# Optimization experiments

Measured on AMD Instinct MI355X. Metric: run time of the kernel, lower is better.

The kernel has to match this reference:

```python
import jax, jax.numpy as jnp
import numpy as np

B, NHID, L, AL = 8, 512, 2048, 4
NHEAD, HEAD_DIM = 8, 64
D = NHEAD * HEAD_DIM
WIN = 3  # unfold_size in the original module
SCALE = 1.0 / float(np.sqrt(HEAD_DIM))


def setup_inputs() -> dict:
    key = jax.random.key(0)
    ks = jax.random.split(key, 6)
    s = 0.02
    return {
        "x": jax.random.normal(ks[0], (B, NHID, L, 1), jnp.float32),
        "ax": jax.random.normal(ks[1], (B, NHID, AL, L), jnp.float32),
        "Wq": jax.random.normal(ks[2], (NHID, D), jnp.float32) * s,
        "bq": jnp.zeros((D,), jnp.float32),
        "Wk": jax.random.normal(ks[3], (NHID, D), jnp.float32) * s,
        "bk": jnp.zeros((D,), jnp.float32),
        "Wv": jax.random.normal(ks[4], (NHID, D), jnp.float32) * s,
        "bv": jnp.zeros((D,), jnp.float32),
        "Wo": jax.random.normal(ks[5], (D, NHID), jnp.float32) * s,
        "bo": jnp.zeros((NHID,), jnp.float32),
    }


def _window_unfold(t):
    # SAME zero-padded sliding window of size 3 along L (== tf.image.extract_patches).
    tp = jnp.pad(t, ((0, 0), (0, 0), (0, 0), (1, 1)))
    Ld = t.shape[-1]
    return jnp.stack([tp[..., i:i + Ld] for i in range(WIN)], axis=3)


def reference(x, ax, Wq, bq, Wk, bk, Wv, bv, Wo, bo):
    # x: [B, nhid, L, 1] -> [B, L, nhid]
    xf = x[..., 0].transpose(0, 2, 1)
    q = (xf @ Wq + bq).transpose(0, 2, 1).reshape(B, NHEAD, HEAD_DIM, L)
    k = (xf @ Wk + bk).transpose(0, 2, 1).reshape(B, NHEAD, HEAD_DIM, L)
    v = (xf @ Wv + bv).transpose(0, 2, 1).reshape(B, NHEAD, HEAD_DIM, L)

    kw = _window_unfold(k)  # [B, nh, hd, 3, L]
    vw = _window_unfold(v)

    # axial context: ax [B, nhid, aL, L] -> [B, aL, L, nhid]
    axf = ax.transpose(0, 2, 3, 1)
    ak = (axf @ Wk + bk).transpose(0, 3, 1, 2).reshape(B, NHEAD, HEAD_DIM, AL, L)
    av = (axf @ Wv + bv).transpose(0, 3, 1, 2).reshape(B, NHEAD, HEAD_DIM, AL, L)

    kall = jnp.concatenate([kw, ak], axis=3)  # [B, nh, hd, 3+aL, L]
    vall = jnp.concatenate([vw, av], axis=3)

    # per-position attention over the (3 + aL) window entries
    scores = jnp.einsum('bndl,bndwl->bnwl', q, kall) * SCALE
    alphas = jax.nn.softmax(scores, axis=2)  # softmax over window dim (dropout omitted)
    att = jnp.einsum('bnwl,bndwl->bndl', alphas, vall).reshape(B, D, L)

    out = att.transpose(0, 2, 1) @ Wo + bo  # [B, L, nhid]
    return out.transpose(0, 2, 1)[..., None]  # [B, nhid, L, 1]
```

## Files before the change

kernel.cpp:

```cpp
#include <hip/hip_runtime.h>
#include <hip/hip_bf16.h>

#define B_ 8
#define NHID_ 512
#define L_ 2048
#define AL_ 4
#define NHEAD_ 8
#define HDIM_ 64
#define D_ 512
#define SCALE_ 0.125f

typedef unsigned short ushort_t;
typedef __attribute__((ext_vector_type(8))) short bf16x8;
typedef __attribute__((ext_vector_type(8))) unsigned short u16x8;
typedef __attribute__((ext_vector_type(4))) float f32x4;

__device__ __forceinline__ float bf2f(ushort_t u) {
  union { unsigned i; float f; } x; x.i = ((unsigned)u) << 16; return x.f;
}
__device__ __forceinline__ ushort_t f2bf(float f) {
  unsigned u = __float_as_uint(f);
  unsigned r = (u + 0x7FFFu + ((u >> 16) & 1u)) >> 16;
  return (ushort_t)r;
}
__device__ __forceinline__ void gload16(const ushort_t* g, ushort_t* l) {
  __builtin_amdgcn_global_load_lds(
      (const __attribute__((address_space(1))) unsigned int*)g,
      (__attribute__((address_space(3))) unsigned int*)l, 16, 0, 0);
}

template <typename Tin>
__global__ __launch_bounds__(256)
void transpose_conv(const Tin* __restrict__ in, ushort_t* __restrict__ out,
                    int R, int C) {
  __shared__ float t[32][33];
  const size_t z = (size_t)blockIdx.z * R * C;
  const int cb = blockIdx.x * 32, rb = blockIdx.y * 32;
  const int tx = threadIdx.x, ty = threadIdx.y;
#pragma unroll
  for (int i = 0; i < 4; i++) {
    const int r = rb + ty + i * 8;
    float v;
    if constexpr (sizeof(Tin) == 4) v = ((const float*)in)[z + (size_t)r * C + cb + tx];
    else                            v = bf2f(((const ushort_t*)in)[z + (size_t)r * C + cb + tx]);
    t[ty + i * 8][tx] = v;
  }
  __syncthreads();
#pragma unroll
  for (int i = 0; i < 4; i++) {
    const int c = cb + ty + i * 8;
    out[z + (size_t)c * R + rb + tx] = f2bf(t[tx][ty + i * 8]);
  }
}

__global__ void prep_bias(const float* __restrict__ bq, const float* __restrict__ bk,
                          const float* __restrict__ bv, float* __restrict__ bcat) {
  const int i = blockIdx.x * 256 + threadIdx.x;
  const float* s = i < 512 ? bq : (i < 1024 ? bk : bv);
  bcat[i] = s[i & 511];
}

template <int OUTF>
__global__ __launch_bounds__(256)
void gemm_mfma(const ushort_t* __restrict__ A, const ushort_t* __restrict__ W,
               const float* __restrict__ bias, void* __restrict__ C0,
               void* __restrict__ C1, void* __restrict__ C2,
               int Ntiles, int MbShift) {
  __shared__ ushort_t lds[8192];
  const int tid = threadIdx.x;
  const int l = tid & 63, w = tid >> 6;

  const int nwg = gridDim.x;
  const int id = (blockIdx.x & 7) * (nwg >> 3) + (blockIdx.x >> 3);
  const int nt = id % Ntiles, mt = id / Ntiles;
  const int bm = mt * 128, bn = nt * 128;

  const ushort_t* gsrc[4];
  ushort_t* ldst[4];
#pragma unroll
  for (int j = 0; j < 4; j++) {
    const int ci = j * 256 + w * 64 + l;
    const int row = (ci & 511) >> 2;
    const int cp = (ci & 3) ^ ((row >> 1) & 3);
    gsrc[j] = (ci < 512 ? A + (size_t)(bm + row) * 512
                        : W + (size_t)(bn + row) * 512) + cp * 8;
    ldst[j] = &lds[j * 2048 + w * 512];
  }

  const int wm = (w & 1) * 64, wn = (w >> 1) * 64;
  int boff[4], aoff[4];
#pragma unroll
  for (int i = 0; i < 4; i++) {
    const int rb = wm + i * 16 + (l & 15);
    boff[i] = rb * 32 + (((l >> 4) ^ ((rb >> 1) & 3)) * 8);
    const int ra = wn + i * 16 + (l & 15);
    aoff[i] = 4096 + ra * 32 + (((l >> 4) ^ ((ra >> 1) & 3)) * 8);
  }

  f32x4 acc[4][4] = {};
  for (int kt = 0; kt < 16; kt++) {
    if (kt) __syncthreads();
#pragma unroll
    for (int j = 0; j < 4; j++) gload16(gsrc[j] + kt * 32, ldst[j]);
    __syncthreads();
    bf16x8 bf[4], af[4];
#pragma unroll
    for (int i = 0; i < 4; i++) bf[i] = *(const bf16x8*)&lds[boff[i]];
#pragma unroll
    for (int i = 0; i < 4; i++) af[i] = *(const bf16x8*)&lds[aoff[i]];
#pragma unroll
    for (int ni = 0; ni < 4; ni++)
#pragma unroll
      for (int mi = 0; mi < 4; mi++)
        acc[ni][mi] = __builtin_amdgcn_mfma_f32_16x16x32_bf16(af[ni], bf[mi],
                                                              acc[ni][mi], 0, 0, 0);
  }

  const int bufi = bn >> 9;
  void* Cb = bufi == 0 ? C0 : (bufi == 1 ? C1 : C2);
  const int nb = bn & 511;
  const int Mb = 1 << MbShift;
#pragma unroll
  for (int ni = 0; ni < 4; ni++) {
#pragma unroll
    for (int r = 0; r < 4; r++) {
      const int tn = wn + ni * 16 + (l >> 4) * 4 + r;
      const float bv = bias[bn + tn];
      const int nl = nb + tn;
#pragma unroll
      for (int mi = 0; mi < 4; mi++) {
        const int m = bm + wm + mi * 16 + (l & 15);
        const int b = m >> MbShift, ml = m & (Mb - 1);
        const size_t idx = (((size_t)b * 512 + nl) << MbShift) + ml;
        const float val = acc[ni][mi][r] + bv;
        if (OUTF) ((float*)Cb)[idx] = val;
        else      ((ushort_t*)Cb)[idx] = f2bf(val);
      }
    }
  }
}

__global__ __launch_bounds__(256)
void attn_win(const ushort_t* __restrict__ q, const ushort_t* __restrict__ k,
              const ushort_t* __restrict__ v, const ushort_t* __restrict__ ak,
              const ushort_t* __restrict__ av, ushort_t* __restrict__ att,
              int b0) {
  const int lane = threadIdx.x & 63;
  const int w    = threadIdx.x >> 6;
  const int dc   = lane & 3;
  const int lc   = lane >> 2;
  const int bb = blockIdx.y >> 3, n = blockIdx.y & 7;
  const int b = b0 + bb;
  const int l8 = blockIdx.x * 512 + w * 128 + lc * 8;
  const int d0 = dc * 16;

  const size_t rq = ((size_t)b * D_ + n * HDIM_ + d0) * L_ + l8;
  const size_t ra = ((size_t)bb * D_ + n * HDIM_ + d0) * (size_t)(AL_ * L_) + l8;
  const ushort_t* qp = q + rq;
  const ushort_t* kp = k + rq;
  const ushort_t* vp = v + rq;
  ushort_t*       op = att + rq;
  const ushort_t* akp = ak + ra;
  const ushort_t* avp = av + ra;

  float s0[8] = {}, s1[8] = {}, s2[8] = {}, s3[8] = {};
  float s4[8] = {}, s5[8] = {}, s6[8] = {};

#pragma unroll 4
  for (int i = 0; i < 16; ++i) {
    const ushort_t* kr = kp + (size_t)i * L_;
    const ushort_t* ar = akp + (size_t)i * (AL_ * L_);
    const u16x8 qv = *(const u16x8*)(qp + (size_t)i * L_);
    const u16x8 kv = *(const u16x8*)kr;
    const u16x8 a0 = *(const u16x8*)(ar);
    const u16x8 a1 = *(const u16x8*)(ar + L_);
    const u16x8 a2 = *(const u16x8*)(ar + 2 * L_);
    const u16x8 a3 = *(const u16x8*)(ar + 3 * L_);
    float qf[8], kf[8];
#pragma unroll
    for (int j = 0; j < 8; ++j) { qf[j] = bf2f(qv[j]); kf[j] = bf2f(kv[j]); }
    float kl = __shfl_up(kf[7], 4);
    if (lc == 0) kl = (l8 > 0) ? bf2f(kr[-1]) : 0.f;
    float kh = __shfl_down(kf[0], 4);
    if (lc == 15) kh = (l8 + 8 < L_) ? bf2f(kr[8]) : 0.f;
#pragma unroll
    for (int j = 0; j < 8; ++j) {
      s0[j] = fmaf(qf[j], j ? kf[j - 1] : kl, s0[j]);
      s1[j] = fmaf(qf[j], kf[j], s1[j]);
      s2[j] = fmaf(qf[j], j < 7 ? kf[j + 1] : kh, s2[j]);
      s3[j] = fmaf(qf[j], bf2f(a0[j]), s3[j]);
      s4[j] = fmaf(qf[j], bf2f(a1[j]), s4[j]);
      s5[j] = fmaf(qf[j], bf2f(a2[j]), s5[j]);
      s6[j] = fmaf(qf[j], bf2f(a3[j]), s6[j]);
    }
  }

#pragma unroll
  for (int j = 0; j < 8; ++j) {
    s0[j] += __shfl_xor(s0[j], 1); s0[j] += __shfl_xor(s0[j], 2);
    s1[j] += __shfl_xor(s1[j], 1); s1[j] += __shfl_xor(s1[j], 2);
    s2[j] += __shfl_xor(s2[j], 1); s2[j] += __shfl_xor(s2[j], 2);
    s3[j] += __shfl_xor(s3[j], 1); s3[j] += __shfl_xor(s3[j], 2);
    s4[j] += __shfl_xor(s4[j], 1); s4[j] += __shfl_xor(s4[j], 2);
    s5[j] += __shfl_xor(s5[j], 1); s5[j] += __shfl_xor(s5[j], 2);
    s6[j] += __shfl_xor(s6[j], 1); s6[j] += __shfl_xor(s6[j], 2);
  }

#pragma unroll
  for (int j = 0; j < 8; ++j) {
    const float t0 = s0[j] * SCALE_, t1 = s1[j] * SCALE_, t2 = s2[j] * SCALE_;
    const float t3 = s3[j] * SCALE_, t4 = s4[j] * SCALE_, t5 = s5[j] * SCALE_;
    const float t6 = s6[j] * SCALE_;
    const float mx = fmaxf(fmaxf(fmaxf(t0, t1), fmaxf(t2, t3)),
                           fmaxf(fmaxf(t4, t5), t6));
    float e0 = __expf(t0 - mx), e1 = __expf(t1 - mx), e2 = __expf(t2 - mx);
    float e3 = __expf(t3 - mx), e4 = __expf(t4 - mx), e5 = __expf(t5 - mx);
    float e6 = __expf(t6 - mx);
    const float inv = 1.f / (e0 + e1 + e2 + e3 + e4 + e5 + e6);
    s0[j] = e0 * inv; s1[j] = e1 * inv; s2[j] = e2 * inv; s3[j] = e3 * inv;
    s4[j] = e4 * inv; s5[j] = e5 * inv; s6[j] = e6 * inv;
  }

#pragma unroll 4
  for (int i = 0; i < 16; ++i) {
    const ushort_t* vr = vp + (size_t)i * L_;
    const ushort_t* ar = avp + (size_t)i * (AL_ * L_);
    const u16x8 vv = *(const u16x8*)vr;
    const u16x8 a0 = *(const u16x8*)(ar);
    const u16x8 a1 = *(const u16x8*)(ar + L_);
    const u16x8 a2 = *(const u16x8*)(ar + 2 * L_);
    const u16x8 a3 = *(const u16x8*)(ar + 3 * L_);
    float vf[8];
#pragma unroll
    for (int j = 0; j < 8; ++j) vf[j] = bf2f(vv[j]);
    float vl = __shfl_up(vf[7], 4);
    if (lc == 0) vl = (l8 > 0) ? bf2f(vr[-1]) : 0.f;
    float vh = __shfl_down(vf[0], 4);
    if (lc == 15) vh = (l8 + 8 < L_) ? bf2f(vr[8]) : 0.f;
    u16x8 o;
#pragma unroll
    for (int j = 0; j < 8; ++j) {
      float r = s0[j] * (j ? vf[j - 1] : vl)
              + s1[j] * vf[j]
              + s2[j] * (j < 7 ? vf[j + 1] : vh);
      r = fmaf(s3[j], bf2f(a0[j]), r);
      r = fmaf(s4[j], bf2f(a1[j]), r);
      r = fmaf(s5[j], bf2f(a2[j]), r);
      r = fmaf(s6[j], bf2f(a3[j]), r);
      o[j] = f2bf(r);
    }
    *(u16x8*)(op + (size_t)i * L_) = o;
  }
}

extern "C" void kernel_launch(void* const* d_in, const int* in_sizes, int n_in,
                              void* d_out, int out_size, void* d_ws, size_t ws_size,
                              hipStream_t stream) {
  const float* x  = (const float*)d_in[0];
  const float* ax = (const float*)d_in[1];
  const float* Wq = (const float*)d_in[2];
  const float* bq = (const float*)d_in[3];
  const float* Wk = (const float*)d_in[4];
  const float* bk = (const float*)d_in[5];
  const float* Wv = (const float*)d_in[6];
  const float* bv = (const float*)d_in[7];
  const float* Wo = (const float*)d_in[8];
  const float* bo = (const float*)d_in[9];
  float* out = (float*)d_out;

  const size_t E  = (size_t)B_ * D_ * L_;
  const size_t EA = (size_t)B_ * D_ * AL_ * L_;
  const size_t CH1 = (size_t)D_ * AL_ * L_;
  const size_t wfix = 1536 * 512 + 512 * 512 + 3072;

  int BCH = 8;
  while (BCH > 1 &&
         (4 * E + EA + 2 * (size_t)BCH * CH1 + wfix) * 2 > ws_size)
    BCH >>= 1;
  const size_t chunkE = (size_t)BCH * CH1;

  ushort_t* wsu = (ushort_t*)d_ws;
  ushort_t* xTb   = wsu;
  ushort_t* qb    = xTb + E;
  ushort_t* kb    = qb + E;
  ushort_t* vb    = kb + E;
  ushort_t* axTb  = vb + E;
  ushort_t* akb   = axTb + EA;
  ushort_t* avb   = akb + chunkE;
  ushort_t* WcatT = avb + chunkE;
  ushort_t* WoT   = WcatT + 1536 * 512;
  float*    bcat  = (float*)(WoT + 512 * 512);
  ushort_t* attb  = xTb;
  ushort_t* attTb = axTb;

  const dim3 t32x8(32, 8);

  transpose_conv<float><<<dim3(16, 16, 1), t32x8, 0, stream>>>(Wq, WcatT, 512, 512);
  transpose_conv<float><<<dim3(16, 16, 1), t32x8, 0, stream>>>(Wk, WcatT + 512 * 512, 512, 512);
  transpose_conv<float><<<dim3(16, 16, 1), t32x8, 0, stream>>>(Wv, WcatT + 1024 * 512, 512, 512);
  transpose_conv<float><<<dim3(16, 16, 1), t32x8, 0, stream>>>(Wo, WoT, 512, 512);
  prep_bias<<<dim3(6), dim3(256), 0, stream>>>(bq, bk, bv, bcat);

  transpose_conv<float><<<dim3(64, 16, B_), t32x8, 0, stream>>>(x, xTb, 512, L_);
  transpose_conv<float><<<dim3(256, 16, B_), t32x8, 0, stream>>>(ax, axTb, 512, AL_ * L_);

  gemm_mfma<0><<<dim3(128 * 12), dim3(256), 0, stream>>>(
      xTb, WcatT, bcat, qb, kb, vb, 12, 11);

  for (int b0 = 0; b0 < B_; b0 += BCH) {
    const ushort_t* axc = axTb + (size_t)b0 * CH1;
    gemm_mfma<0><<<dim3(BCH * 64 * 8), dim3(256), 0, stream>>>(
        axc, WcatT + 512 * 512, bcat + 512, akb, avb, nullptr, 8, 13);
    attn_win<<<dim3(L_ / 512, BCH * NHEAD_), dim3(256), 0, stream>>>(
        qb, kb, vb, akb, avb, attb, b0);
  }

  transpose_conv<ushort_t><<<dim3(64, 16, B_), t32x8, 0, stream>>>(attb, attTb, 512, L_);

  gemm_mfma<1><<<dim3(128 * 4), dim3(256), 0, stream>>>(
      attTb, WoT, bo, out, nullptr, nullptr, 4, 11);
}
```

Baseline: 498.4 us.

## Fuse input transposes into GEMM A-loads with double-buffered LDS pipeline

The GEMM now reads fp32 activations in their original [nhid, L] layout, converts them to bf16 in registers and writes them to LDS. This removes the separate transpose passes over x, ax (the large one) and the attention output. The main loop is double-buffered: A and W loads for the next k-tile are issued while MFMAs run on the current one. The attention kernel now writes fp32 output directly, so the Wo GEMM consumes it without a bf16 transpose. The cost is strided per-column scalar global loads for A and more LDS per block, which may lower occupancy.

New measurement: 564.4 us. +13.2%, slower.

```diff
diff --git a/kernel.cpp b/kernel.cpp
--- a/kernel.cpp
+++ b/kernel.cpp
@@ -29,9 +29,8 @@
       (__attribute__((address_space(3))) unsigned int*)l, 16, 0, 0);
 }
 
-template <typename Tin>
 __global__ __launch_bounds__(256)
-void transpose_conv(const Tin* __restrict__ in, ushort_t* __restrict__ out,
+void transpose_conv(const float* __restrict__ in, ushort_t* __restrict__ out,
                     int R, int C) {
   __shared__ float t[32][33];
   const size_t z = (size_t)blockIdx.z * R * C;
@@ -40,10 +39,7 @@
 #pragma unroll
   for (int i = 0; i < 4; i++) {
     const int r = rb + ty + i * 8;
-    float v;
-    if constexpr (sizeof(Tin) == 4) v = ((const float*)in)[z + (size_t)r * C + cb + tx];
-    else                            v = bf2f(((const ushort_t*)in)[z + (size_t)r * C + cb + tx]);
-    t[ty + i * 8][tx] = v;
+    t[ty + i * 8][tx] = in[z + (size_t)r * C + cb + tx];
   }
   __syncthreads();
 #pragma unroll
@@ -62,11 +58,11 @@
 
 template <int OUTF>
 __global__ __launch_bounds__(256)
-void gemm_mfma(const ushort_t* __restrict__ A, const ushort_t* __restrict__ W,
-               const float* __restrict__ bias, void* __restrict__ C0,
-               void* __restrict__ C1, void* __restrict__ C2,
-               int Ntiles, int MbShift) {
-  __shared__ ushort_t lds[8192];
+void gemm_fa(const float* __restrict__ A, const ushort_t* __restrict__ W,
+             const float* __restrict__ bias, void* __restrict__ C0,
+             void* __restrict__ C1, void* __restrict__ C2,
+             int M, long long sA, long long sC, int Ntiles) {
+  __shared__ ushort_t lds[16384];
   const int tid = threadIdx.x;
   const int l = tid & 63, w = tid >> 6;
 
@@ -74,17 +70,22 @@
   const int id = (blockIdx.x & 7) * (nwg >> 3) + (blockIdx.x >> 3);
   const int nt = id % Ntiles, mt = id / Ntiles;
   const int bm = mt * 128, bn = nt * 128;
-
-  const ushort_t* gsrc[4];
-  ushort_t* ldst[4];
-#pragma unroll
-  for (int j = 0; j < 4; j++) {
-    const int ci = j * 256 + w * 64 + l;
-    const int row = (ci & 511) >> 2;
-    const int cp = (ci & 3) ^ ((row >> 1) & 3);
-    gsrc[j] = (ci < 512 ? A + (size_t)(bm + row) * 512
-                        : W + (size_t)(bn + row) * 512) + cp * 8;
-    ldst[j] = &lds[j * 2048 + w * 512];
+  const float* Ab = A + (size_t)blockIdx.z * sA + bm;
+
+  const int am = tid & 127;
+  const int ao0 = tid >> 7, ao1 = (tid >> 7) + 2;
+  const int awr0 = am * 32 + ((ao0 ^ ((am >> 1) & 3)) * 8);
+  const int awr1 = am * 32 + ((ao1 ^ ((am >> 1) & 3)) * 8);
+
+  const ushort_t* wsrc[2];
+  int wdoff[2];
+#pragma unroll
+  for (int j = 0; j < 2; j++) {
+    const int cw = j * 256 + w * 64 + l;
+    const int row = cw >> 2;
+    const int cp = (cw & 3) ^ ((row >> 1) & 3);
+    wsrc[j] = W + (size_t)(bn + row) * 512 + cp * 8;
+    wdoff[j] = 4096 + j * 2048 + w * 512;
   }
 
   const int wm = (w & 1) * 64, wn = (w >> 1) * 64;
@@ -97,29 +98,64 @@
     aoff[i] = 4096 + ra * 32 + (((l >> 4) ^ ((ra >> 1) & 3)) * 8);
   }
 
+  float fa0[8], fa1[8];
+#define LOAD_A(kt)                                                        \
+  {                                                                       \
+    const float* s0_ = Ab + (size_t)((kt) * 32 + ao0 * 8) * M + am;       \
+    const float* s1_ = Ab + (size_t)((kt) * 32 + ao1 * 8) * M + am;       \
+    _Pragma("unroll") for (int j = 0; j < 8; j++) {                       \
+      fa0[j] = s0_[(size_t)j * M];                                        \
+      fa1[j] = s1_[(size_t)j * M];                                        \
+    }                                                                     \
+  }
+#define LOAD_W(kt, buf)                                                   \
+  {                                                                       \
+    _Pragma("unroll") for (int j = 0; j < 2; j++)                         \
+        gload16(wsrc[j] + (kt) * 32, &lds[(buf) * 8192 + wdoff[j]]);      \
+  }
+#define WRITE_A(buf)                                                      \
+  {                                                                       \
+    bf16x8 p0_, p1_;                                                      \
+    _Pragma("unroll") for (int j = 0; j < 8; j++) {                       \
+      p0_[j] = (short)f2bf(fa0[j]);                                       \
+      p1_[j] = (short)f2bf(fa1[j]);                                       \
+    }                                                                     \
+    *(bf16x8*)&lds[(buf) * 8192 + awr0] = p0_;                            \
+    *(bf16x8*)&lds[(buf) * 8192 + awr1] = p1_;                            \
+  }
+
+  LOAD_A(0);
+  LOAD_W(0, 0);
+  WRITE_A(0);
+  __syncthreads();
+
   f32x4 acc[4][4] = {};
+  int cur = 0;
   for (int kt = 0; kt < 16; kt++) {
-    if (kt) __syncthreads();
-#pragma unroll
-    for (int j = 0; j < 4; j++) gload16(gsrc[j] + kt * 32, ldst[j]);
-    __syncthreads();
+    if (kt < 15) {
+      LOAD_A(kt + 1);
+      LOAD_W(kt + 1, cur ^ 1);
+    }
+    const int cb = cur * 8192;
     bf16x8 bf[4], af[4];
 #pragma unroll
-    for (int i = 0; i < 4; i++) bf[i] = *(const bf16x8*)&lds[boff[i]];
-#pragma unroll
-    for (int i = 0; i < 4; i++) af[i] = *(const bf16x8*)&lds[aoff[i]];
+    for (int i = 0; i < 4; i++) bf[i] = *(const bf16x8*)&lds[cb + boff[i]];
+#pragma unroll
+    for (int i = 0; i < 4; i++) af[i] = *(const bf16x8*)&lds[cb + aoff[i]];
 #pragma unroll
     for (int ni = 0; ni < 4; ni++)
 #pragma unroll
       for (int mi = 0; mi < 4; mi++)
         acc[ni][mi] = __builtin_amdgcn_mfma_f32_16x16x32_bf16(af[ni], bf[mi],
                                                               acc[ni][mi], 0, 0, 0);
+    if (kt < 15) WRITE_A(cur ^ 1);
+    __syncthreads();
+    cur ^= 1;
   }
 
   const int bufi = bn >> 9;
   void* Cb = bufi == 0 ? C0 : (bufi == 1 ? C1 : C2);
   const int nb = bn & 511;
-  const int Mb = 1 << MbShift;
 #pragma unroll
   for (int ni = 0; ni < 4; ni++) {
 #pragma unroll
@@ -130,20 +166,22 @@
 #pragma unroll
       for (int mi = 0; mi < 4; mi++) {
         const int m = bm + wm + mi * 16 + (l & 15);
-        const int b = m >> MbShift, ml = m & (Mb - 1);
-        const size_t idx = (((size_t)b * 512 + nl) << MbShift) + ml;
+        const size_t idx = (size_t)blockIdx.z * sC + (size_t)nl * M + m;
         const float val = acc[ni][mi][r] + bv;
         if (OUTF) ((float*)Cb)[idx] = val;
         else      ((ushort_t*)Cb)[idx] = f2bf(val);
       }
     }
   }
+#undef LOAD_A
+#undef LOAD_W
+#undef WRITE_A
 }
 
 __global__ __launch_bounds__(256)
 void attn_win(const ushort_t* __restrict__ q, const ushort_t* __restrict__ k,
               const ushort_t* __restrict__ v, const ushort_t* __restrict__ ak,
-              const ushort_t* __restrict__ av, ushort_t* __restrict__ att,
+              const ushort_t* __restrict__ av, float* __restrict__ att,
               int b0) {
   const int lane = threadIdx.x & 63;
   const int w    = threadIdx.x >> 6;
@@ -159,7 +197,7 @@
   const ushort_t* qp = q + rq;
   const ushort_t* kp = k + rq;
   const ushort_t* vp = v + rq;
-  ushort_t*       op = att + rq;
+  float*          op = att + rq;
   const ushort_t* akp = ak + ra;
   const ushort_t* avp = av + ra;
 
@@ -237,7 +275,7 @@
     if (lc == 0) vl = (l8 > 0) ? bf2f(vr[-1]) : 0.f;
     float vh = __shfl_down(vf[0], 4);
     if (lc == 15) vh = (l8 + 8 < L_) ? bf2f(vr[8]) : 0.f;
-    u16x8 o;
+    f32x4 olo, ohi;
 #pragma unroll
     for (int j = 0; j < 8; ++j) {
       float r = s0[j] * (j ? vf[j - 1] : vl)
@@ -247,9 +285,10 @@
       r = fmaf(s4[j], bf2f(a1[j]), r);
       r = fmaf(s5[j], bf2f(a2[j]), r);
       r = fmaf(s6[j], bf2f(a3[j]), r);
-      o[j] = f2bf(r);
+      if (j < 4) olo[j] = r; else ohi[j - 4] = r;
     }
-    *(u16x8*)(op + (size_t)i * L_) = o;
+    *(f32x4*)(op + (size_t)i * L_) = olo;
+    *(f32x4*)(op + (size_t)i * L_ + 4) = ohi;
   }
 }
 
@@ -268,55 +307,48 @@
   const float* bo = (const float*)d_in[9];
   float* out = (float*)d_out;
 
-  const size_t E  = (size_t)B_ * D_ * L_;
-  const size_t EA = (size_t)B_ * D_ * AL_ * L_;
+  const size_t E   = (size_t)B_ * D_ * L_;
   const size_t CH1 = (size_t)D_ * AL_ * L_;
   const size_t wfix = 1536 * 512 + 512 * 512 + 3072;
 
   int BCH = 8;
-  while (BCH > 1 &&
-         (4 * E + EA + 2 * (size_t)BCH * CH1 + wfix) * 2 > ws_size)
+  while (BCH > 1 && (5 * E + 2 * (size_t)BCH * CH1 + wfix) * 2 > ws_size)
     BCH >>= 1;
   const size_t chunkE = (size_t)BCH * CH1;
 
   ushort_t* wsu = (ushort_t*)d_ws;
-  ushort_t* xTb   = wsu;
-  ushort_t* qb    = xTb + E;
+  ushort_t* qb    = wsu;
   ushort_t* kb    = qb + E;
   ushort_t* vb    = kb + E;
-  ushort_t* axTb  = vb + E;
-  ushort_t* akb   = axTb + EA;
+  float*    attf  = (float*)(vb + E);
+  ushort_t* akb   = vb + E + 2 * E;
   ushort_t* avb   = akb + chunkE;
   ushort_t* WcatT = avb + chunkE;
   ushort_t* WoT   = WcatT + 1536 * 512;
   float*    bcat  = (float*)(WoT + 512 * 512);
-  ushort_t* attb  = xTb;
-  ushort_t* attTb = axTb;
 
   const dim3 t32x8(32, 8);
 
-  transpose_conv<float><<<dim3(16, 16, 1), t32x8, 0, stream>>>(Wq, WcatT, 512, 512);
-  transpose_conv<float><<<dim3(16, 16, 1), t32x8, 0, stream>>>(Wk, WcatT + 512 * 512, 512, 512);
-  transpose_conv<float><<<dim3(16, 16, 1), t32x8, 0, stream>>>(Wv, WcatT + 1024 * 512, 512, 512);
-  transpose_conv<float><<<dim3(16, 16, 1), t32x8, 0, stream>>>(Wo, WoT, 512, 512);
+  transpose_conv<<<dim3(16, 16, 1), t32x8, 0, stream>>>(Wq, WcatT, 512, 512);
+  transpose_conv<<<dim3(16, 16, 1), t32x8, 0, stream>>>(Wk, WcatT + 512 * 512, 512, 512);
+  transpose_conv<<<dim3(16, 16, 1), t32x8, 0, stream>>>(Wv, WcatT + 1024 * 512, 512, 512);
+  transpose_conv<<<dim3(16, 16, 1), t32x8, 0, stream>>>(Wo, WoT, 512, 512);
   prep_bias<<<dim3(6), dim3(256), 0, stream>>>(bq, bk, bv, bcat);
 
-  transpose_conv<float><<<dim3(64, 16, B_), t32x8, 0, stream>>>(x, xTb, 512, L_);
-  transpose_conv<float><<<dim3(256, 16, B_), t32x8, 0, stream>>>(ax, axTb, 512, AL_ * L_);
-
-  gemm_mfma<0><<<dim3(128 * 12), dim3(256), 0, stream>>>(
-      xTb, WcatT, bcat, qb, kb, vb, 12, 11);
+  gemm_fa<0><<<dim3(16 * 12, 1, B_), dim3(256), 0, stream>>>(
+      x, WcatT, bcat, qb, kb, vb,
+      L_, (long long)NHID_ * L_, (long long)D_ * L_, 12);
 
   for (int b0 = 0; b0 < B_; b0 += BCH) {
-    const ushort_t* axc = axTb + (size_t)b0 * CH1;
-    gemm_mfma<0><<<dim3(BCH * 64 * 8), dim3(256), 0, stream>>>(
-        axc, WcatT + 512 * 512, bcat + 512, akb, avb, nullptr, 8, 13);
+    const float* axc = ax + (size_t)b0 * NHID_ * AL_ * L_;
+    gemm_fa<0><<<dim3(64 * 8, 1, BCH), dim3(256), 0, stream>>>(
+        axc, WcatT + 512 * 512, bcat + 512, akb, avb, nullptr,
+        AL_ * L_, (long long)NHID_ * AL_ * L_, (long long)CH1, 8);
     attn_win<<<dim3(L_ / 512, BCH * NHEAD_), dim3(256), 0, stream>>>(
-        qb, kb, vb, akb, avb, attb, b0);
-  }
-
-  transpose_conv<ushort_t><<<dim3(64, 16, B_), t32x8, 0, stream>>>(attb, attTb, 512, L_);
-
-  gemm_mfma<1><<<dim3(128 * 4), dim3(256), 0, stream>>>(
-      attTb, WoT, bo, out, nullptr, nullptr, 4, 11);
-}
+        qb, kb, vb, akb, avb, attf, b0);
+  }
+
+  gemm_fa<1><<<dim3(16 * 4, 1, B_), dim3(256), 0, stream>>>(
+      attf, WoT, bo, out, nullptr, nullptr,
+      L_, (long long)D_ * L_, (long long)NHID_ * L_, 4);
+}
```

## Merge prep kernels, vectorize 64x64 transposes, fuse QKV and axial GEMMs

Applied to the files above, without the earlier changes.

Folds the four weight transposes and the bias copy into one launch. Replaces the 32x32 scalar transposes with 64x64 tiles that use float4 loads and 4-wide bf16 stores, and handles x and ax in a single launch. When the whole batch fits in the workspace, the QKV projection and the axial K/V projection run as one dual-problem GEMM launch, followed by one attention launch. This cuts launch count and tail effects, and makes the memory-bound transposes more efficient, at the cost of branchier kernels and more LDS bank conflicts in the transposed read.

Result: faster. 478.7 us (-4.0%).

```diff
diff --git a/kernel.cpp b/kernel.cpp
--- a/kernel.cpp
+++ b/kernel.cpp
@@ -13,6 +13,7 @@
 typedef unsigned short ushort_t;
 typedef __attribute__((ext_vector_type(8))) short bf16x8;
 typedef __attribute__((ext_vector_type(8))) unsigned short u16x8;
+typedef __attribute__((ext_vector_type(4))) unsigned short u16x4;
 typedef __attribute__((ext_vector_type(4))) float f32x4;
 
 __device__ __forceinline__ float bf2f(ushort_t u) {
@@ -29,49 +30,126 @@
       (__attribute__((address_space(3))) unsigned int*)l, 16, 0, 0);
 }
 
-template <typename Tin>
 __global__ __launch_bounds__(256)
-void transpose_conv(const Tin* __restrict__ in, ushort_t* __restrict__ out,
-                    int R, int C) {
-  __shared__ float t[32][33];
-  const size_t z = (size_t)blockIdx.z * R * C;
-  const int cb = blockIdx.x * 32, rb = blockIdx.y * 32;
+void wprep(const float* __restrict__ Wq, const float* __restrict__ Wk,
+           const float* __restrict__ Wv, const float* __restrict__ Wo,
+           const float* __restrict__ bq, const float* __restrict__ bk,
+           const float* __restrict__ bv, ushort_t* __restrict__ WcatT,
+           ushort_t* __restrict__ WoT, float* __restrict__ bcat) {
+  const int bid = blockIdx.x;
   const int tx = threadIdx.x, ty = threadIdx.y;
+  if (bid == 1024) {
+    const int t = ty * 32 + tx;
+    for (int i = t; i < 1536; i += 256) {
+      const float* s = i < 512 ? bq : (i < 1024 ? bk : bv);
+      bcat[i] = s[i & 511];
+    }
+    return;
+  }
+  __shared__ float tl[32][33];
+  const int wi = bid >> 8;
+  const float* src = wi == 0 ? Wq : wi == 1 ? Wk : wi == 2 ? Wv : Wo;
+  ushort_t* dst = wi == 0 ? WcatT : wi == 1 ? WcatT + 512 * 512
+                : wi == 2 ? WcatT + 1024 * 512 : WoT;
+  const int r = bid & 255;
+  const int cb = (r & 15) * 32, rb = (r >> 4) * 32;
+#pragma unroll
+  for (int i = 0; i < 4; i++)
+    tl[ty + i * 8][tx] = src[(size_t)(rb + ty + i * 8) * 512 + cb + tx];
+  __syncthreads();
+#pragma unroll
+  for (int i = 0; i < 4; i++)
+    dst[(size_t)(cb + ty + i * 8) * 512 + rb + tx] = f2bf(tl[tx][ty + i * 8]);
+}
+
+__global__ __launch_bounds__(256)
+void trans64_in(const float* __restrict__ x, ushort_t* __restrict__ xT,
+                const float* __restrict__ ax, ushort_t* __restrict__ axT) {
+  __shared__ ushort_t tl[64][68];
+  int id = blockIdx.x;
+  const float* in; ushort_t* out; int C, z, rt, ct;
+  if (id < 2048) {
+    in = x; out = xT; C = 2048;
+    z = id >> 8; const int r = id & 255; ct = r & 31; rt = r >> 5;
+  } else {
+    id -= 2048;
+    in = ax; out = axT; C = 8192;
+    z = id >> 10; const int r = id & 1023; ct = r & 127; rt = r >> 7;
+  }
+  const int rb = rt * 64, cb = ct * 64;
+  const int t = threadIdx.x;
+  const int cx = t & 15, ry = t >> 4;
 #pragma unroll
   for (int i = 0; i < 4; i++) {
-    const int r = rb + ty + i * 8;
-    float v;
-    if constexpr (sizeof(Tin) == 4) v = ((const float*)in)[z + (size_t)r * C + cb + tx];
-    else                            v = bf2f(((const ushort_t*)in)[z + (size_t)r * C + cb + tx]);
-    t[ty + i * 8][tx] = v;
+    const int rl = ry + i * 16;
+    const float4 v = *(const float4*)&in[((size_t)z * 512 + rb + rl) * C + cb + cx * 4];
+    u16x4 u; u[0] = f2bf(v.x); u[1] = f2bf(v.y); u[2] = f2bf(v.z); u[3] = f2bf(v.w);
+    *(u16x4*)&tl[rl][cx * 4] = u;
   }
   __syncthreads();
+  const int rx = t & 15, cy = t >> 4;
 #pragma unroll
   for (int i = 0; i < 4; i++) {
-    const int c = cb + ty + i * 8;
-    out[z + (size_t)c * R + rb + tx] = f2bf(t[tx][ty + i * 8]);
-  }
-}
-
-__global__ void prep_bias(const float* __restrict__ bq, const float* __restrict__ bk,
-                          const float* __restrict__ bv, float* __restrict__ bcat) {
-  const int i = blockIdx.x * 256 + threadIdx.x;
-  const float* s = i < 512 ? bq : (i < 1024 ? bk : bv);
-  bcat[i] = s[i & 511];
+    const int cl = cy + i * 16;
+    u16x4 u;
+#pragma unroll
+    for (int j = 0; j < 4; j++) u[j] = tl[rx * 4 + j][cl];
+    *(u16x4*)&out[((size_t)z * C + cb + cl) * 512 + rb + rx * 4] = u;
+  }
+}
+
+__global__ __launch_bounds__(256)
+void trans64_bf(const ushort_t* __restrict__ in, ushort_t* __restrict__ out) {
+  __shared__ ushort_t tl[64][68];
+  const int id = blockIdx.x;
+  const int z = id >> 8; const int r = id & 255;
+  const int ct = r & 31, rt = r >> 5;
+  const int rb = rt * 64, cb = ct * 64;
+  const int t = threadIdx.x;
+  const int cx = t & 15, ry = t >> 4;
+#pragma unroll
+  for (int i = 0; i < 4; i++) {
+    const int rl = ry + i * 16;
+    const u16x4 v = *(const u16x4*)&in[((size_t)z * 512 + rb + rl) * 2048 + cb + cx * 4];
+    *(u16x4*)&tl[rl][cx * 4] = v;
+  }
+  __syncthreads();
+  const int rx = t & 15, cy = t >> 4;
+#pragma unroll
+  for (int i = 0; i < 4; i++) {
+    const int cl = cy + i * 16;
+    u16x4 u;
+#pragma unroll
+    for (int j = 0; j < 4; j++) u[j] = tl[rx * 4 + j][cl];
+    *(u16x4*)&out[((size_t)z * 2048 + cb + cl) * 512 + rb + rx * 4] = u;
+  }
 }
 
 template <int OUTF>
 __global__ __launch_bounds__(256)
-void gemm_mfma(const ushort_t* __restrict__ A, const ushort_t* __restrict__ W,
-               const float* __restrict__ bias, void* __restrict__ C0,
-               void* __restrict__ C1, void* __restrict__ C2,
-               int Ntiles, int MbShift) {
+void gemm_dual(const ushort_t* __restrict__ A0, const ushort_t* __restrict__ W0,
+               const float* __restrict__ bias0, void* C00, void* C01, void* C02,
+               int Nt0, int Ms0, int tiles0,
+               const ushort_t* __restrict__ A1, const ushort_t* __restrict__ W1,
+               const float* __restrict__ bias1, void* C10, void* C11,
+               int Nt1, int Ms1) {
   __shared__ ushort_t lds[8192];
   const int tid = threadIdx.x;
   const int l = tid & 63, w = tid >> 6;
 
   const int nwg = gridDim.x;
-  const int id = (blockIdx.x & 7) * (nwg >> 3) + (blockIdx.x >> 3);
+  int id = (blockIdx.x & 7) * (nwg >> 3) + (blockIdx.x >> 3);
+
+  const ushort_t* A; const ushort_t* W; const float* bias;
+  void *Cp0, *Cp1, *Cp2; int Ntiles, MbShift;
+  if (id < tiles0) {
+    A = A0; W = W0; bias = bias0; Cp0 = C00; Cp1 = C01; Cp2 = C02;
+    Ntiles = Nt0; MbShift = Ms0;
+  } else {
+    id -= tiles0;
+    A = A1; W = W1; bias = bias1; Cp0 = C10; Cp1 = C11; Cp2 = nullptr;
+    Ntiles = Nt1; MbShift = Ms1;
+  }
   const int nt = id % Ntiles, mt = id / Ntiles;
   const int bm = mt * 128, bn = nt * 128;
 
@@ -117,9 +195,8 @@
   }
 
   const int bufi = bn >> 9;
-  void* Cb = bufi == 0 ? C0 : (bufi == 1 ? C1 : C2);
+  void* Cb = bufi == 0 ? Cp0 : (bufi == 1 ? Cp1 : Cp2);
   const int nb = bn & 511;
-  const int Mb = 1 << MbShift;
 #pragma unroll
   for (int ni = 0; ni < 4; ni++) {
 #pragma unroll
@@ -130,7 +207,7 @@
 #pragma unroll
       for (int mi = 0; mi < 4; mi++) {
         const int m = bm + wm + mi * 16 + (l & 15);
-        const int b = m >> MbShift, ml = m & (Mb - 1);
+        const int b = m >> MbShift, ml = m & ((1 << MbShift) - 1);
         const size_t idx = (((size_t)b * 512 + nl) << MbShift) + ml;
         const float val = acc[ni][mi][r] + bv;
         if (OUTF) ((float*)Cb)[idx] = val;
@@ -293,30 +370,34 @@
   ushort_t* attb  = xTb;
   ushort_t* attTb = axTb;
 
-  const dim3 t32x8(32, 8);
-
-  transpose_conv<float><<<dim3(16, 16, 1), t32x8, 0, stream>>>(Wq, WcatT, 512, 512);
-  transpose_conv<float><<<dim3(16, 16, 1), t32x8, 0, stream>>>(Wk, WcatT + 512 * 512, 512, 512);
-  transpose_conv<float><<<dim3(16, 16, 1), t32x8, 0, stream>>>(Wv, WcatT + 1024 * 512, 512, 512);
-  transpose_conv<float><<<dim3(16, 16, 1), t32x8, 0, stream>>>(Wo, WoT, 512, 512);
-  prep_bias<<<dim3(6), dim3(256), 0, stream>>>(bq, bk, bv, bcat);
-
-  transpose_conv<float><<<dim3(64, 16, B_), t32x8, 0, stream>>>(x, xTb, 512, L_);
-  transpose_conv<float><<<dim3(256, 16, B_), t32x8, 0, stream>>>(ax, axTb, 512, AL_ * L_);
-
-  gemm_mfma<0><<<dim3(128 * 12), dim3(256), 0, stream>>>(
-      xTb, WcatT, bcat, qb, kb, vb, 12, 11);
-
-  for (int b0 = 0; b0 < B_; b0 += BCH) {
-    const ushort_t* axc = axTb + (size_t)b0 * CH1;
-    gemm_mfma<0><<<dim3(BCH * 64 * 8), dim3(256), 0, stream>>>(
-        axc, WcatT + 512 * 512, bcat + 512, akb, avb, nullptr, 8, 13);
-    attn_win<<<dim3(L_ / 512, BCH * NHEAD_), dim3(256), 0, stream>>>(
-        qb, kb, vb, akb, avb, attb, b0);
-  }
-
-  transpose_conv<ushort_t><<<dim3(64, 16, B_), t32x8, 0, stream>>>(attb, attTb, 512, L_);
-
-  gemm_mfma<1><<<dim3(128 * 4), dim3(256), 0, stream>>>(
-      attTb, WoT, bo, out, nullptr, nullptr, 4, 11);
-}
+  wprep<<<dim3(1025), dim3(32, 8), 0, stream>>>(Wq, Wk, Wv, Wo, bq, bk, bv,
+                                                WcatT, WoT, bcat);
+
+  trans64_in<<<dim3(2048 + 8192), dim3(256), 0, stream>>>(x, xTb, ax, axTb);
+
+  if (BCH == 8) {
+    gemm_dual<0><<<dim3(1536 + 4096), dim3(256), 0, stream>>>(
+        xTb, WcatT, bcat, qb, kb, vb, 12, 11, 1536,
+        axTb, WcatT + 512 * 512, bcat + 512, akb, avb, 8, 13);
+    attn_win<<<dim3(L_ / 512, B_ * NHEAD_), dim3(256), 0, stream>>>(
+        qb, kb, vb, akb, avb, attb, 0);
+  } else {
+    gemm_dual<0><<<dim3(1536), dim3(256), 0, stream>>>(
+        xTb, WcatT, bcat, qb, kb, vb, 12, 11, 1536,
+        xTb, WcatT, bcat, qb, kb, 12, 11);
+    for (int b0 = 0; b0 < B_; b0 += BCH) {
+      const ushort_t* axc = axTb + (size_t)b0 * CH1;
+      gemm_dual<0><<<dim3(BCH * 512), dim3(256), 0, stream>>>(
+          axc, WcatT + 512 * 512, bcat + 512, akb, avb, nullptr, 8, 13, 0,
+          axc, WcatT + 512 * 512, bcat + 512, akb, avb, 8, 13);
+      attn_win<<<dim3(L_ / 512, BCH * NHEAD_), dim3(256), 0, stream>>>(
+          qb, kb, vb, akb, avb, attb, b0);
+    }
+  }
+
+  trans64_bf<<<dim3(2048), dim3(256), 0, stream>>>(attb, attTb);
+
+  gemm_dual<1><<<dim3(512), dim3(256), 0, stream>>>(
+      attTb, WoT, bo, out, nullptr, nullptr, 4, 11, 512,
+      attTb, WoT, bo, out, nullptr, 4, 11);
+}
```
